# Kernel optimization log

Measured on AMD Instinct MI355X. Metric: run time of the kernel, lower is better.

The kernel has to match this reference:

```python
import jax, jax.numpy as jnp
import numpy as np

N = 100000
E = 1600000
IN, HID, OUT = 128, 256, 128


def setup_inputs() -> dict:
    key = jax.random.key(0)
    ks = jax.random.split(key, 8)
    x = jax.random.normal(ks[0], (N, IN), dtype=jnp.float32)
    edge_index = jax.random.randint(ks[1], (2, E), 0, N, dtype=jnp.int64)
    # PyG SAGEConv params: lin_l (neighbor aggr, with bias), lin_r (root, no bias)
    def glorot(k, shape):
        fan_in = shape[1]
        return jax.random.normal(k, shape, dtype=jnp.float32) / jnp.sqrt(jnp.float32(fan_in))
    W1l = glorot(ks[2], (HID, IN)); b1 = jnp.zeros((HID,), jnp.float32)
    W1r = glorot(ks[3], (HID, IN))
    W2l = glorot(ks[4], (OUT, HID)); b2 = jnp.zeros((OUT,), jnp.float32)
    W2r = glorot(ks[5], (OUT, HID))
    return {"x": x, "edge_index": edge_index, "W1l": W1l, "b1": b1,
            "W1r": W1r, "W2l": W2l, "b2": b2, "W2r": W2r}


def sage_conv(x, row, col, Wl, b, Wr, n_nodes):
    # mean-aggregate neighbor features x[row] at target nodes col
    msg = x[row]                                               # [E, d]
    s = jax.ops.segment_sum(msg, col, num_segments=n_nodes)    # [N, d]
    deg = jax.ops.segment_sum(jnp.ones((row.shape[0], 1), x.dtype), col,
                              num_segments=n_nodes)            # [N, 1]
    mean = s / jnp.maximum(deg, 1.0)
    return mean @ Wl.T + b + x @ Wr.T


def reference(x, edge_index, W1l, b1, W1r, W2l, b2, W2r):
    row, col = edge_index[0], edge_index[1]
    h = sage_conv(x, row, col, W1l, b1, W1r, N)
    h = jax.nn.relu(h)
    # dropout is identity in eval mode
    out = sage_conv(h, row, col, W2l, b2, W2r, N)
    return out
```

## Files before the change

kernel.cpp:

```cpp
#include <hip/hip_runtime.h>
#include <hip/hip_bf16.h>
#include <hip/hip_fp16.h>

#define NN 100000
#define NE 1600000
#define NCHUNK ((NN + 127) / 128)
#define NPB 512
#define NB 256
#define CHUNK 8192
#define NCH ((NE + CHUNK - 1) / CHUNK)

typedef __attribute__((ext_vector_type(8))) short short8;
typedef __attribute__((ext_vector_type(4))) float float4v;
typedef __attribute__((ext_vector_type(2))) float float2v;

__device__ __forceinline__ unsigned short f2bf(float f) {
    unsigned int b = __float_as_uint(f);
    return (unsigned short)((b + 0x7fffu + ((b >> 16) & 1u)) >> 16);
}
__device__ __forceinline__ unsigned int pack_bf16(float lo, float hi) {
    return (unsigned int)f2bf(lo) | ((unsigned int)f2bf(hi) << 16);
}
__device__ __forceinline__ void addp8(float* a, uint2 u) {
    float2v f;
    f = __builtin_amdgcn_cvt_pk_f32_fp8(u.x, false); a[0] += f.x; a[1] += f.y;
    f = __builtin_amdgcn_cvt_pk_f32_fp8(u.x, true);  a[2] += f.x; a[3] += f.y;
    f = __builtin_amdgcn_cvt_pk_f32_fp8(u.y, false); a[4] += f.x; a[5] += f.y;
    f = __builtin_amdgcn_cvt_pk_f32_fp8(u.y, true);  a[6] += f.x; a[7] += f.y;
}
__device__ __forceinline__ unsigned char f2fp8(float v) {
    int r = __builtin_amdgcn_cvt_pk_fp8_f32(v, v, 0, false);
    return (unsigned char)(r & 0xff);
}
__device__ __forceinline__ unsigned short pack2fp8(float lo, float hi) {
    int r = __builtin_amdgcn_cvt_pk_fp8_f32(lo, hi, 0, false);
    return (unsigned short)(r & 0xffff);
}
__device__ __forceinline__ float h2f(unsigned short u) {
    return __half2float(__ushort_as_half(u));
}

__global__ void k_prep(const float* x, const float* W1l, const float* W1r,
                       const float* W2l, const float* W2r, const int* ei,
                       unsigned int* axb_u, unsigned short* xf8, unsigned short* wb1,
                       unsigned short* wb2, int* bcnt) {
    __shared__ int hh[NB];
    int b = blockIdx.x, t = threadIdx.x;
    if (b < 25000) {
        int tt = b * 256 + t;
        int node = tt >> 6, i = tt & 63;
        float2 v = ((const float2*)x)[tt];
        axb_u[(size_t)node * 128 + 64 + i] = pack_bf16(v.x, v.y);
        xf8[(size_t)node * 64 + i] = pack2fp8(v.x, v.y);
    } else if (b < 25128) {
        int i = (b - 25000) * 256 + t;
        int r1 = i >> 7, c1 = i & 127;
        wb1[r1 * 256 + c1]       = f2bf(W1l[i]);
        wb1[r1 * 256 + 128 + c1] = f2bf(W1r[i]);
        wb2[i]         = f2bf(W2l[i]);
        wb2[32768 + i] = f2bf(W2r[i]);
    } else {
        hh[t] = 0;
        __syncthreads();
        int e0 = (b - 25128) * 6250;
        for (int e = e0 + t; e < e0 + 6250; e += 256)
            atomicAdd(&hh[ei[NE + e] >> 9], 1);
        __syncthreads();
        if (hh[t]) atomicAdd(&bcnt[t], hh[t]);
    }
}

__global__ void k_bscan(const int* bcnt, int* boff, int* bcur) {
    __shared__ int s[NB];
    int t = threadIdx.x;
    int v = bcnt[t];
    s[t] = v;
    __syncthreads();
    for (int d = 1; d < NB; d <<= 1) {
        int val = (t >= d) ? s[t - d] : 0;
        __syncthreads();
        s[t] += val;
        __syncthreads();
    }
    boff[t + 1] = s[t];
    if (t == 0) boff[0] = 0;
    bcur[t] = s[t] - v;
}

__global__ __launch_bounds__(256) void k_bscatter(const int* ei, int* bcur, unsigned int* pairs) {
    __shared__ unsigned int buf[CHUNK];
    __shared__ int cnt[NB];
    __shared__ int lbase[NB];
    __shared__ int lcur[NB];
    __shared__ int gpos[NB];
    int t = threadIdx.x;
    int e0 = blockIdx.x * CHUNK;
    int nedge = NE - e0; if (nedge > CHUNK) nedge = CHUNK;
    cnt[t] = 0;
    __syncthreads();
    for (int i = t; i < nedge; i += 256)
        atomicAdd(&cnt[ei[NE + e0 + i] >> 9], 1);
    __syncthreads();
    int v = cnt[t];
    lcur[t] = v;
    __syncthreads();
    for (int d = 1; d < NB; d <<= 1) {
        int val = (t >= d) ? lcur[t - d] : 0;
        __syncthreads();
        lcur[t] += val;
        __syncthreads();
    }
    lbase[t] = lcur[t] - v;
    gpos[t] = atomicAdd(&bcur[t], v);
    __syncthreads();
    lcur[t] = lbase[t];
    __syncthreads();
    for (int i = t; i < nedge; i += 256) {
        int r = ei[e0 + i], c = ei[NE + e0 + i];
        int b = c >> 9;
        int p = atomicAdd(&lcur[b], 1);
        buf[p] = (unsigned)r | ((unsigned)(c & 511) << 17);
    }
    __syncthreads();
    int wv = t >> 6, lane = t & 63;
    for (int b = wv; b < NB; b += 4) {
        int n = cnt[b], lb = lbase[b], gp = gpos[b];
        for (int i = lane; i < n; i += 64)
            pairs[gp + i] = buf[lb + i];
    }
}

__global__ __launch_bounds__(256) void k_build(const unsigned int* pairs, const int* boff,
                                               int* off, int* deg, int* csr) {
    __shared__ int ldeg[NPB];
    __shared__ int lcur[NPB];
    __shared__ int sscan[256];
    int b = blockIdx.x;
    int nbase = b * NPB;
    if (nbase >= NN) return;
    int t = threadIdx.x;
    int base = boff[b], cntb = boff[b + 1] - base;
    ldeg[t] = 0; ldeg[t + 256] = 0;
    __syncthreads();
    for (int i = t; i < cntb; i += 256) {
        unsigned int pr = pairs[base + i];
        atomicAdd(&ldeg[pr >> 17], 1);
    }
    __syncthreads();
    int d0 = ldeg[2 * t], d1 = ldeg[2 * t + 1];
    int v = d0 + d1;
    sscan[t] = v;
    __syncthreads();
    for (int d = 1; d < 256; d <<= 1) {
        int val = (t >= d) ? sscan[t - d] : 0;
        __syncthreads();
        sscan[t] += val;
        __syncthreads();
    }
    int ex = sscan[t] - v;
    lcur[2 * t] = ex; lcur[2 * t + 1] = ex + d0;
    __syncthreads();
    int nloc = NN - nbase; if (nloc > NPB) nloc = NPB;
    for (int ln = t; ln < nloc; ln += 256) {
        off[nbase + ln] = base + lcur[ln];
        deg[nbase + ln] = ldeg[ln];
    }
    __syncthreads();
    for (int i = t; i < cntb; i += 256) {
        unsigned int pr = pairs[base + i];
        int p = atomicAdd(&lcur[pr >> 17], 1);
        csr[base + p] = (int)(pr & 0x1FFFFu);
    }
}

__global__ void k_agg1(const uint2* xf8, const int* off, const int* deg,
                       const int* csr, unsigned int* axb_w) {
    int wid = (blockIdx.x * 256 + threadIdx.x) >> 6;
    if (wid >= NN) return;
    int lane = threadIdx.x & 63;
    int sub = lane >> 4, l16 = lane & 15;
    int start = off[wid], d = deg[wid];
    const uint2* gp = xf8 + l16;
    float a[8] = {0.f, 0.f, 0.f, 0.f, 0.f, 0.f, 0.f, 0.f};
    int j = sub;
    for (; j + 4 < d; j += 8) {
        int n0 = csr[start + j];
        int n1 = csr[start + j + 4];
        uint2 u0 = gp[(size_t)n0 * 16];
        uint2 u1 = gp[(size_t)n1 * 16];
        addp8(a, u0); addp8(a, u1);
    }
    if (j < d) {
        int nb = csr[start + j];
        uint2 u = gp[(size_t)nb * 16];
        addp8(a, u);
    }
#pragma unroll
    for (int i = 0; i < 8; i++) {
        a[i] += __shfl_xor(a[i], 16, 64);
        a[i] += __shfl_xor(a[i], 32, 64);
    }
    if (sub == 0) {
        float inv = 1.0f / (float)(d > 0 ? d : 1);
        uint4 o;
        o.x = pack_bf16(a[0] * inv, a[1] * inv);
        o.y = pack_bf16(a[2] * inv, a[3] * inv);
        o.z = pack_bf16(a[4] * inv, a[5] * inv);
        o.w = pack_bf16(a[6] * inv, a[7] * inv);
        *(uint4*)(axb_w + (size_t)wid * 128 + (l16 << 2)) = o;
    }
}

__global__ void k_agg2(const uint2* g, const int* off, const int* deg,
                       const int* csr, const unsigned short* partial, float* out) {
    int wid = (blockIdx.x * 256 + threadIdx.x) >> 6;
    if (wid >= NN) return;
    int lane = threadIdx.x & 63;
    int sub = lane >> 4, l16 = lane & 15;
    int start = off[wid], d = deg[wid];
    const uint2* gp = g + l16;
    float a[8] = {0.f, 0.f, 0.f, 0.f, 0.f, 0.f, 0.f, 0.f};
    int j = sub;
    for (; j + 4 < d; j += 8) {
        int n0 = csr[start + j];
        int n1 = csr[start + j + 4];
        uint2 u0 = gp[(size_t)n0 * 16];
        uint2 u1 = gp[(size_t)n1 * 16];
        addp8(a, u0); addp8(a, u1);
    }
    if (j < d) {
        int nb = csr[start + j];
        uint2 u = gp[(size_t)nb * 16];
        addp8(a, u);
    }
#pragma unroll
    for (int i = 0; i < 8; i++) {
        a[i] += __shfl_xor(a[i], 16, 64);
        a[i] += __shfl_xor(a[i], 32, 64);
    }
    if (sub == 0) {
        float inv = 1.0f / (float)(d > 0 ? d : 1);
        uint4 pu = *(const uint4*)(partial + (size_t)wid * 128 + (l16 << 3));
        float4 c0, c1;
        c0.x = h2f(pu.x & 0xffff) + a[0] * inv; c0.y = h2f(pu.x >> 16) + a[1] * inv;
        c0.z = h2f(pu.y & 0xffff) + a[2] * inv; c0.w = h2f(pu.y >> 16) + a[3] * inv;
        c1.x = h2f(pu.z & 0xffff) + a[4] * inv; c1.y = h2f(pu.z >> 16) + a[5] * inv;
        c1.z = h2f(pu.w & 0xffff) + a[6] * inv; c1.w = h2f(pu.w >> 16) + a[7] * inv;
        float4* po = (float4*)(out + (size_t)wid * 128) + (l16 << 1);
        po[0] = c0; po[1] = c1;
    }
}

__global__ __launch_bounds__(256, 1) void k_gemm1(const unsigned short* A, const unsigned short* wb,
                                                  const float* b1, unsigned short* H) {
    __shared__ unsigned short Bs[256 * 256];
    int t = threadIdx.x;
    {
        const short8* src = (const short8*)wb;
        short8* dst = (short8*)Bs;
#pragma unroll
        for (int i = 0; i < 32; i++) dst[i * 256 + t] = src[i * 256 + t];
    }
    __syncthreads();
    int wv = t >> 6, lane = t & 63;
    int mrow = lane & 15, quad = lane >> 4;
    float bias[16];
#pragma unroll
    for (int ct = 0; ct < 16; ct++) bias[ct] = b1[ct * 16 + mrow];
    for (int chunk = blockIdx.x; chunk < NCHUNK; chunk += gridDim.x) {
        int base = chunk * 128 + wv * 32;
        if (base >= NN) continue;
        short8 afr[2][8];
#pragma unroll
        for (int kk = 0; kk < 8; kk++) {
            afr[0][kk] = *(const short8*)(A + (size_t)(base + mrow) * 256 + kk * 32 + quad * 8);
            afr[1][kk] = *(const short8*)(A + (size_t)(base + 16 + mrow) * 256 + kk * 32 + quad * 8);
        }
        float4v acc[2][16];
#pragma unroll
        for (int h = 0; h < 2; h++)
#pragma unroll
            for (int ct = 0; ct < 16; ct++) acc[h][ct] = (float4v)(0.0f);
#pragma unroll
        for (int kk = 0; kk < 8; kk++) {
            int koff = kk * 32 + quad * 8;
#pragma unroll
            for (int ct = 0; ct < 16; ct++) {
                short8 b = *(const short8*)(Bs + (ct * 16 + mrow) * 256 + koff);
                acc[0][ct] = __builtin_amdgcn_mfma_f32_16x16x32_bf16(afr[0][kk], b, acc[0][ct], 0, 0, 0);
                acc[1][ct] = __builtin_amdgcn_mfma_f32_16x16x32_bf16(afr[1][kk], b, acc[1][ct], 0, 0, 0);
            }
        }
#pragma unroll
        for (int ct = 0; ct < 16; ct++) {
            int col = ct * 16 + mrow;
#pragma unroll
            for (int h = 0; h < 2; h++)
#pragma unroll
                for (int r = 0; r < 4; r++) {
                    int node = base + h * 16 + quad * 4 + r;
                    float v = acc[h][ct][r] + bias[ct];
                    H[(size_t)node * 256 + col] = f2bf(fmaxf(v, 0.f));
                }
        }
    }
}

__global__ __launch_bounds__(256, 1) void k_gemm2(const unsigned short* A, const unsigned short* wb,
                                                  const float* b2, unsigned char* g,
                                                  unsigned short* partial) {
    __shared__ unsigned short Bs[256 * 256];
    int t = threadIdx.x;
    {
        const short8* src = (const short8*)wb;
        short8* dst = (short8*)Bs;
#pragma unroll
        for (int i = 0; i < 32; i++) dst[i * 256 + t] = src[i * 256 + t];
    }
    __syncthreads();
    int wv = t >> 6, lane = t & 63;
    int mrow = lane & 15, quad = lane >> 4;
    float bias[8];
#pragma unroll
    for (int i = 0; i < 8; i++) bias[i] = b2[i * 16 + mrow];
    for (int chunk = blockIdx.x; chunk < NCHUNK; chunk += gridDim.x) {
        int base = chunk * 128 + wv * 32;
        if (base >= NN) continue;
        short8 afr[2][8];
#pragma unroll
        for (int kk = 0; kk < 8; kk++) {
            afr[0][kk] = *(const short8*)(A + (size_t)(base + mrow) * 256 + kk * 32 + quad * 8);
            afr[1][kk] = *(const short8*)(A + (size_t)(base + 16 + mrow) * 256 + kk * 32 + quad * 8);
        }
        float4v acc[2][16];
#pragma unroll
        for (int h = 0; h < 2; h++)
#pragma unroll
            for (int ct = 0; ct < 16; ct++) acc[h][ct] = (float4v)(0.0f);
#pragma unroll
        for (int kk = 0; kk < 8; kk++) {
            int koff = kk * 32 + quad * 8;
#pragma unroll
            for (int ct = 0; ct < 16; ct++) {
                short8 b = *(const short8*)(Bs + (ct * 16 + mrow) * 256 + koff);
                acc[0][ct] = __builtin_amdgcn_mfma_f32_16x16x32_bf16(afr[0][kk], b, acc[0][ct], 0, 0, 0);
                acc[1][ct] = __builtin_amdgcn_mfma_f32_16x16x32_bf16(afr[1][kk], b, acc[1][ct], 0, 0, 0);
            }
        }
#pragma unroll
        for (int ct = 0; ct < 16; ct++) {
            int col = ct * 16 + mrow;
#pragma unroll
            for (int h = 0; h < 2; h++)
#pragma unroll
                for (int r = 0; r < 4; r++) {
                    int node = base + h * 16 + quad * 4 + r;
                    float v = acc[h][ct][r];
                    if (ct < 8) {
                        g[(size_t)node * 128 + col] = f2fp8(v);
                    } else {
                        __half hf = __float2half(v + bias[ct - 8]);
                        partial[(size_t)node * 128 + (col - 128)] = __half_as_ushort(hf);
                    }
                }
        }
    }
}

extern "C" void kernel_launch(void* const* d_in, const int* in_sizes, int n_in,
                              void* d_out, int out_size, void* d_ws, size_t ws_size,
                              hipStream_t stream) {
    const float* x   = (const float*)d_in[0];
    const int*   ei  = (const int*)d_in[1];
    const float* W1l = (const float*)d_in[2];
    const float* b1  = (const float*)d_in[3];
    const float* W1r = (const float*)d_in[4];
    const float* W2l = (const float*)d_in[5];
    const float* b2  = (const float*)d_in[6];
    const float* W2r = (const float*)d_in[7];
    float* out = (float*)d_out;

    char* p = (char*)d_ws;
    unsigned int* axb = (unsigned int*)p; p += (size_t)NN * 256 * 2;
    unsigned short* h = (unsigned short*)p; p += (size_t)NN * 256 * 2;
    unsigned char* g  = (unsigned char*)p; p += (size_t)NN * 128;
    unsigned short* xf8 = (unsigned short*)p; p += (size_t)NN * 128;
    unsigned short* wb1 = (unsigned short*)p; p += 65536 * 2;
    unsigned short* wb2 = (unsigned short*)p; p += 65536 * 2;
    int* deg  = (int*)p; p += (size_t)NN * 4;
    int* off  = (int*)p; p += (size_t)NN * 4;
    int* csr  = (int*)p; p += (size_t)NE * 4;
    int* bcnt = (int*)p; p += NB * 4;
    int* boff = (int*)p; p += (NB + 1) * 4;
    int* bcur = (int*)p; p += NB * 4;
    if (ws_size < (size_t)(p - (char*)d_ws)) return;
    unsigned int* pairs = (unsigned int*)h;
    unsigned short* partial = (unsigned short*)axb;

    hipMemsetAsync(bcnt, 0, NB * 4, stream);
    k_prep<<<25384, 256, 0, stream>>>(x, W1l, W1r, W2l, W2r, ei, axb, xf8, wb1, wb2, bcnt);
    k_bscan<<<1, NB, 0, stream>>>(bcnt, boff, bcur);
    k_bscatter<<<NCH, 256, 0, stream>>>(ei, bcur, pairs);
    k_build<<<NB, 256, 0, stream>>>(pairs, boff, off, deg, csr);
    k_agg1<<<NN * 64 / 256, 256, 0, stream>>>((const uint2*)xf8, off, deg, csr, axb);
    k_gemm1<<<256, 256, 0, stream>>>((const unsigned short*)axb, wb1, b1, h);
    k_gemm2<<<256, 256, 0, stream>>>(h, wb2, b2, g, partial);
    k_agg2<<<25000, 256, 0, stream>>>((const uint2*)g, off, deg, csr, partial, out);
}
```

Measured before the change: 364.3 us.

## Split GEMM output columns across blocks with padded LDS weight tiles

Both dense GEMM kernels change from 256 persistent blocks, each holding the full 256x256 weight in LDS, to one block per (row chunk, 64-column group). Each block stages only a 64-row slice of the weights, padded to a 264-element row stride so LDS reads avoid bank conflicts, and keeps fewer accumulators so occupancy can rise to 4 blocks per CU. The intent is to cut the large serial weight-load prologue and register pressure and to expose more parallelism. The cost is that every A row tile is now read four times from global memory/L2, and the weight slice is reloaded per block.

```diff
diff --git a/kernel.cpp b/kernel.cpp
--- a/kernel.cpp
+++ b/kernel.cpp
@@ -251,117 +251,130 @@
     }
 }
 
-__global__ __launch_bounds__(256, 1) void k_gemm1(const unsigned short* A, const unsigned short* wb,
+#define BROW 264
+__global__ __launch_bounds__(256, 4) void k_gemm1(const unsigned short* A, const unsigned short* wb,
                                                   const float* b1, unsigned short* H) {
-    __shared__ unsigned short Bs[256 * 256];
+    __shared__ unsigned short Bs[64 * BROW];
     int t = threadIdx.x;
+    int cg = blockIdx.x & 3, chunk = blockIdx.x >> 2;
     {
-        const short8* src = (const short8*)wb;
+        const short8* src = (const short8*)(wb + (size_t)cg * 64 * 256);
         short8* dst = (short8*)Bs;
 #pragma unroll
-        for (int i = 0; i < 32; i++) dst[i * 256 + t] = src[i * 256 + t];
+        for (int i = 0; i < 8; i++) {
+            int gi = i * 256 + t;
+            int r = gi >> 5, c = gi & 31;
+            dst[r * 33 + c] = src[gi];
+        }
     }
     __syncthreads();
     int wv = t >> 6, lane = t & 63;
     int mrow = lane & 15, quad = lane >> 4;
-    float bias[16];
-#pragma unroll
-    for (int ct = 0; ct < 16; ct++) bias[ct] = b1[ct * 16 + mrow];
-    for (int chunk = blockIdx.x; chunk < NCHUNK; chunk += gridDim.x) {
-        int base = chunk * 128 + wv * 32;
-        if (base >= NN) continue;
-        short8 afr[2][8];
-#pragma unroll
-        for (int kk = 0; kk < 8; kk++) {
-            afr[0][kk] = *(const short8*)(A + (size_t)(base + mrow) * 256 + kk * 32 + quad * 8);
-            afr[1][kk] = *(const short8*)(A + (size_t)(base + 16 + mrow) * 256 + kk * 32 + quad * 8);
-        }
-        float4v acc[2][16];
+    int base = chunk * 128 + wv * 32;
+    if (base >= NN) return;
+    float bias[4];
+#pragma unroll
+    for (int ctl = 0; ctl < 4; ctl++) bias[ctl] = b1[cg * 64 + ctl * 16 + mrow];
+    float4v acc[2][4];
+#pragma unroll
+    for (int h = 0; h < 2; h++)
+#pragma unroll
+        for (int ctl = 0; ctl < 4; ctl++) acc[h][ctl] = (float4v)(0.0f);
+    const short8* a0p = (const short8*)(A + (size_t)(base + mrow) * 256);
+    const short8* a1p = (const short8*)(A + (size_t)(base + 16 + mrow) * 256);
+#pragma unroll
+    for (int kk = 0; kk < 8; kk++) {
+        short8 a0 = a0p[kk * 4 + quad];
+        short8 a1 = a1p[kk * 4 + quad];
+        int koff = kk * 32 + quad * 8;
+#pragma unroll
+        for (int ctl = 0; ctl < 4; ctl++) {
+            short8 b = *(const short8*)(Bs + (ctl * 16 + mrow) * BROW + koff);
+            acc[0][ctl] = __builtin_amdgcn_mfma_f32_16x16x32_bf16(a0, b, acc[0][ctl], 0, 0, 0);
+            acc[1][ctl] = __builtin_amdgcn_mfma_f32_16x16x32_bf16(a1, b, acc[1][ctl], 0, 0, 0);
+        }
+    }
+#pragma unroll
+    for (int ctl = 0; ctl < 4; ctl++) {
+        int col = cg * 64 + ctl * 16 + mrow;
 #pragma unroll
         for (int h = 0; h < 2; h++)
 #pragma unroll
-            for (int ct = 0; ct < 16; ct++) acc[h][ct] = (float4v)(0.0f);
-#pragma unroll
-        for (int kk = 0; kk < 8; kk++) {
-            int koff = kk * 32 + quad * 8;
-#pragma unroll
-            for (int ct = 0; ct < 16; ct++) {
-                short8 b = *(const short8*)(Bs + (ct * 16 + mrow) * 256 + koff);
-                acc[0][ct] = __builtin_amdgcn_mfma_f32_16x16x32_bf16(afr[0][kk], b, acc[0][ct], 0, 0, 0);
-                acc[1][ct] = __builtin_amdgcn_mfma_f32_16x16x32_bf16(afr[1][kk], b, acc[1][ct], 0, 0, 0);
+            for (int r = 0; r < 4; r++) {
+                int node = base + h * 16 + quad * 4 + r;
+                float v = acc[h][ctl][r] + bias[ctl];
+                H[(size_t)node * 256 + col] = f2bf(fmaxf(v, 0.f));
             }
-        }
-#pragma unroll
-        for (int ct = 0; ct < 16; ct++) {
-            int col = ct * 16 + mrow;
+    }
+}
+
+__global__ __launch_bounds__(256, 4) void k_gemm2(const unsigned short* A, const unsigned short* wb,
+                                                  const float* b2, unsigned char* g,
+                                                  unsigned short* partial) {
+    __shared__ unsigned short Bs[64 * BROW];
+    int t = threadIdx.x;
+    int cg = blockIdx.x & 3, chunk = blockIdx.x >> 2;
+    {
+        const short8* src = (const short8*)(wb + (size_t)cg * 64 * 256);
+        short8* dst = (short8*)Bs;
+#pragma unroll
+        for (int i = 0; i < 8; i++) {
+            int gi = i * 256 + t;
+            int r = gi >> 5, c = gi & 31;
+            dst[r * 33 + c] = src[gi];
+        }
+    }
+    __syncthreads();
+    int wv = t >> 6, lane = t & 63;
+    int mrow = lane & 15, quad = lane >> 4;
+    int base = chunk * 128 + wv * 32;
+    if (base >= NN) return;
+    float bias[4];
+#pragma unroll
+    for (int ctl = 0; ctl < 4; ctl++)
+        bias[ctl] = (cg >= 2) ? b2[cg * 64 + ctl * 16 + mrow - 128] : 0.f;
+    float4v acc[2][4];
+#pragma unroll
+    for (int h = 0; h < 2; h++)
+#pragma unroll
+        for (int ctl = 0; ctl < 4; ctl++) acc[h][ctl] = (float4v)(0.0f);
+    const short8* a0p = (const short8*)(A + (size_t)(base + mrow) * 256);
+    const short8* a1p = (const short8*)(A + (size_t)(base + 16 + mrow) * 256);
+#pragma unroll
+    for (int kk = 0; kk < 8; kk++) {
+        short8 a0 = a0p[kk * 4 + quad];
+        short8 a1 = a1p[kk * 4 + quad];
+        int koff = kk * 32 + quad * 8;
+#pragma unroll
+        for (int ctl = 0; ctl < 4; ctl++) {
+            short8 b = *(const short8*)(Bs + (ctl * 16 + mrow) * BROW + koff);
+            acc[0][ctl] = __builtin_amdgcn_mfma_f32_16x16x32_bf16(a0, b, acc[0][ctl], 0, 0, 0);
+            acc[1][ctl] = __builtin_amdgcn_mfma_f32_16x16x32_bf16(a1, b, acc[1][ctl], 0, 0, 0);
+        }
+    }
+    if (cg < 2) {
+#pragma unroll
+        for (int ctl = 0; ctl < 4; ctl++) {
+            int col = cg * 64 + ctl * 16 + mrow;
 #pragma unroll
             for (int h = 0; h < 2; h++)
 #pragma unroll
                 for (int r = 0; r < 4; r++) {
                     int node = base + h * 16 + quad * 4 + r;
-                    float v = acc[h][ct][r] + bias[ct];
-                    H[(size_t)node * 256 + col] = f2bf(fmaxf(v, 0.f));
+                    g[(size_t)node * 128 + col] = f2fp8(acc[h][ctl][r]);
                 }
         }
-    }
-}
-
-__global__ __launch_bounds__(256, 1) void k_gemm2(const unsigned short* A, const unsigned short* wb,
-                                                  const float* b2, unsigned char* g,
-                                                  unsigned short* partial) {
-    __shared__ unsigned short Bs[256 * 256];
-    int t = threadIdx.x;
-    {
-        const short8* src = (const short8*)wb;
-        short8* dst = (short8*)Bs;
-#pragma unroll
-        for (int i = 0; i < 32; i++) dst[i * 256 + t] = src[i * 256 + t];
-    }
-    __syncthreads();
-    int wv = t >> 6, lane = t & 63;
-    int mrow = lane & 15, quad = lane >> 4;
-    float bias[8];
-#pragma unroll
-    for (int i = 0; i < 8; i++) bias[i] = b2[i * 16 + mrow];
-    for (int chunk = blockIdx.x; chunk < NCHUNK; chunk += gridDim.x) {
-        int base = chunk * 128 + wv * 32;
-        if (base >= NN) continue;
-        short8 afr[2][8];
-#pragma unroll
-        for (int kk = 0; kk < 8; kk++) {
-            afr[0][kk] = *(const short8*)(A + (size_t)(base + mrow) * 256 + kk * 32 + quad * 8);
-            afr[1][kk] = *(const short8*)(A + (size_t)(base + 16 + mrow) * 256 + kk * 32 + quad * 8);
-        }
-        float4v acc[2][16];
-#pragma unroll
-        for (int h = 0; h < 2; h++)
-#pragma unroll
-            for (int ct = 0; ct < 16; ct++) acc[h][ct] = (float4v)(0.0f);
-#pragma unroll
-        for (int kk = 0; kk < 8; kk++) {
-            int koff = kk * 32 + quad * 8;
-#pragma unroll
-            for (int ct = 0; ct < 16; ct++) {
-                short8 b = *(const short8*)(Bs + (ct * 16 + mrow) * 256 + koff);
-                acc[0][ct] = __builtin_amdgcn_mfma_f32_16x16x32_bf16(afr[0][kk], b, acc[0][ct], 0, 0, 0);
-                acc[1][ct] = __builtin_amdgcn_mfma_f32_16x16x32_bf16(afr[1][kk], b, acc[1][ct], 0, 0, 0);
-            }
-        }
-#pragma unroll
-        for (int ct = 0; ct < 16; ct++) {
-            int col = ct * 16 + mrow;
+    } else {
+#pragma unroll
+        for (int ctl = 0; ctl < 4; ctl++) {
+            int pcol = cg * 64 + ctl * 16 + mrow - 128;
 #pragma unroll
             for (int h = 0; h < 2; h++)
 #pragma unroll
                 for (int r = 0; r < 4; r++) {
                     int node = base + h * 16 + quad * 4 + r;
-                    float v = acc[h][ct][r];
-                    if (ct < 8) {
-                        g[(size_t)node * 128 + col] = f2fp8(v);
-                    } else {
-                        __half hf = __float2half(v + bias[ct - 8]);
-                        partial[(size_t)node * 128 + (col - 128)] = __half_as_ushort(hf);
-                    }
+                    __half hf = __float2half(acc[h][ctl][r] + bias[ctl]);
+                    partial[(size_t)node * 128 + pcol] = __half_as_ushort(hf);
                 }
         }
     }
@@ -403,7 +416,7 @@
     k_bscatter<<<NCH, 256, 0, stream>>>(ei, bcur, pairs);
     k_build<<<NB, 256, 0, stream>>>(pairs, boff, off, deg, csr);
     k_agg1<<<NN * 64 / 256, 256, 0, stream>>>((const uint2*)xf8, off, deg, csr, axb);
-    k_gemm1<<<256, 256, 0, stream>>>((const unsigned short*)axb, wb1, b1, h);
-    k_gemm2<<<256, 256, 0, stream>>>(h, wb2, b2, g, partial);
+    k_gemm1<<<NCHUNK * 4, 256, 0, stream>>>((const unsigned short*)axb, wb1, b1, h);
+    k_gemm2<<<NCHUNK * 4, 256, 0, stream>>>(h, wb2, b2, g, partial);
     k_agg2<<<25000, 256, 0, stream>>>((const uint2*)g, off, deg, csr, partial, out);
 }
```

Result: slower. 373.3 us (+2.5%).
